# Kernel tuning notes

Hardware: AMD Instinct MI355X
Metric: run time of the kernel (lower is better)

## Reference

```python
import jax, jax.numpy as jnp
import numpy as np

SIZE = 784          # number of MPS sites (pixels)
D = 32              # bond dimension
EMB_D = 2           # local feature dim, embedding x -> [1-x, x]
NUM_LABELS = 10
LABEL_SITE = SIZE // 2
BATCH = 128
INIT_STD = 0.01     # matches default 'random_eye' init


def setup_inputs() -> dict:
    key = jax.random.key(0)
    k1, k2, k3 = jax.random.split(key, 3)
    # raw pixel values in [0,1] so the affine embedding is valid
    batch_input = jax.random.uniform(k1, (BATCH, SIZE), dtype=jnp.float32)
    eye = jnp.eye(D, dtype=jnp.float32)
    # 'random_eye' init: identity (broadcast over site & physical dims) + small noise.
    # Keeps the 784-long matrix chain numerically well-conditioned.
    core_tensors = eye[None, :, None, :] + INIT_STD * jax.random.normal(
        k2, (SIZE, D, EMB_D, D), dtype=jnp.float32)
    label_tensor = eye[:, None, :] + INIT_STD * jax.random.normal(
        k3, (D, NUM_LABELS, D), dtype=jnp.float32)
    return {"batch_input": batch_input,
            "core_tensors": core_tensors,
            "label_tensor": label_tensor}


def _chain_matmul(mats):
    """Ordered product M_0 @ M_1 @ ... @ M_{n-1} via log-depth pairwise tree.
    mats: [B, n, D, D] -> [B, D, D]. n is static, so the Python while is fine."""
    while mats.shape[1] > 1:
        n = mats.shape[1]
        half = n // 2
        prod = jnp.matmul(mats[:, 0:2 * half:2], mats[:, 1:2 * half:2])
        if n % 2:
            prod = jnp.concatenate([prod, mats[:, -1:]], axis=1)
        mats = prod
    return mats[:, 0]


def reference(batch_input, core_tensors, label_tensor):
    # embedding_map: x -> [1-x, x]                                  [B, S, d]
    emb = jnp.stack([1.0 - batch_input, batch_input], axis=-1)
    # _contract_batch_input: per-site matrices M[b,s] = sum_d core[s,:,d,:]*emb[b,s,d]
    mats = jnp.einsum('sadc,bsd->bsac', core_tensors, emb)       # [B, S, D, D]
    left = _chain_matmul(mats[:, :LABEL_SITE])                    # [B, D, D]
    right = _chain_matmul(mats[:, LABEL_SITE:])                   # [B, D, D]
    # periodic bc: out[b,l] = trace(left @ T_l @ right)
    return jnp.einsum('bij,jlk,bki->bl', left, label_tensor, right)  # [B, num_labels]
```

## Files before the change

kernel.cpp:

```cpp
#include <hip/hip_runtime.h>
#include <stdint.h>

typedef float f32x16 __attribute__((ext_vector_type(16)));
typedef short bf16x8 __attribute__((ext_vector_type(8)));
typedef uint32_t u32;
typedef uint32_t u32x4 __attribute__((ext_vector_type(4)));

#define SIZE 784
#define NLBL 10
#define LABEL_SITE 392
#define BATCH 128
#define PRE_ELEMS (SIZE * 2 * 64 * 4)

#if defined(__has_builtin)
#if __has_builtin(__builtin_amdgcn_permlane32_swap)
#define HAVE_PLSWAP 1
#endif
#endif
#ifndef HAVE_PLSWAP
#define HAVE_PLSWAP 0
#endif


__device__ inline u32 cvt_pk(float a, float b) {
  u32 r;
  asm("v_cvt_pk_bf16_f32 %0, %1, %2" : "=v"(r) : "v"(a), "v"(b));
  return r;
}
__device__ inline float lo16f(u32 h) { return __uint_as_float(h << 16); }
__device__ inline float hi16f(u32 h) { return __uint_as_float(h & 0xffff0000u); }

__device__ inline void split_pack(const float s[8], u32 hi[4], u32 lo[4]) {
#pragma unroll
  for (int p = 0; p < 4; ++p) {
    u32 h = cvt_pk(s[2 * p], s[2 * p + 1]);
    hi[p] = h;
    lo[p] = cvt_pk(s[2 * p] - lo16f(h), s[2 * p + 1] - hi16f(h));
  }
}

__device__ inline f32x16 mfma_bb(const u32 (&a)[4], const u32 (&b)[4], f32x16 c) {
  union U { u32 u[4]; bf16x8 v; };
  U A, B;
#pragma unroll
  for (int i = 0; i < 4; ++i) { A.u[i] = a[i]; B.u[i] = b[i]; }
  return __builtin_amdgcn_mfma_f32_32x32x16_bf16(A.v, B.v, c, 0, 0, 0);
}
__device__ inline f32x16 mfma_v4(u32x4 a, const u32 (&b)[4], f32x16 c) {
  union UA { u32x4 u; bf16x8 v; } A; A.u = a;
  union UB { u32 u[4]; bf16x8 v; } B;
#pragma unroll
  for (int i = 0; i < 4; ++i) B.u[i] = b[i];
  return __builtin_amdgcn_mfma_f32_32x32x16_bf16(A.v, B.v, c, 0, 0, 0);
}

__device__ inline f32x16 ident_acc(int lane) {
  const int gam = lane & 31, hib = lane >> 5;
  f32x16 a;
#pragma unroll
  for (int reg = 0; reg < 16; ++reg) {
    int rho = (reg & 3) + 8 * (reg >> 2) + 4 * hib;
    a[reg] = (rho == gam) ? 1.0f : 0.0f;
  }
  return a;
}

__device__ inline int probe_mode(int lane) {
#if HAVE_PLSWAP
  u32 a = (u32)lane, b = (u32)(64 + lane);
  auto r = __builtin_amdgcn_permlane32_swap(a, b, false, false);
  u32 eLo = (u32)(lane + (lane & 32));
  u32 eHi = (u32)(lane + 32 + (lane & 32));
  if (__all(r[0] == eLo) && __all(r[1] == eHi)) return 1;
  if (__all(r[0] == eHi) && __all(r[1] == eLo)) return 2;
#endif
  return 0;
}

template <int MODE>
__device__ inline void build_b(const f32x16& acc, int hib, int t,
                               u32 (&Bh)[4], u32 (&Bl)[4]) {
  float slot[8];
#pragma unroll
  for (int j = 0; j < 4; ++j) {
    const int q1 = 8 * t + j, q2 = q1 + 4;
#if HAVE_PLSWAP
    if (MODE != 0) {
      u32 au = __float_as_uint(acc[q1]), bu = __float_as_uint(acc[q2]);
      auto r = __builtin_amdgcn_permlane32_swap(au, bu, false, false);
      slot[j]     = __uint_as_float(MODE == 1 ? r[0] : r[1]);
      slot[j + 4] = __uint_as_float(MODE == 1 ? r[1] : r[0]);
    } else
#endif
    {
      float z = hib ? acc[q1] : acc[q2];
      float wv = __shfl_xor(z, 32, 64);
      slot[j]     = hib ? wv : acc[q1];
      slot[j + 4] = hib ? acc[q2] : wv;
    }
  }
  split_pack(slot, Bh, Bl);
}

template <int MODE>
__device__ inline f32x16 chain_step(const u32 (&Ah)[2][4], const u32 (&Al)[2][4],
                                    f32x16 acc, int hib) {
  f32x16 r;
#pragma unroll
  for (int q = 0; q < 16; ++q) r[q] = 0.0f;
#pragma unroll
  for (int t = 0; t < 2; ++t) {
    u32 Bh[4], Bl[4];
    build_b<MODE>(acc, hib, t, Bh, Bl);
    r = mfma_bb(Al[t], Bh, r);
    r = mfma_bb(Ah[t], Bl, r);
    r = mfma_bb(Ah[t], Bh, r);
  }
  return r;
}

__device__ inline void store_cd(float* dst, f32x16 acc, int lane) {
  const int gam = lane & 31, hib = lane >> 5;
#pragma unroll
  for (int reg = 0; reg < 16; ++reg) {
    int rho = (reg & 3) + 8 * (reg >> 2) + 4 * hib;
    dst[rho * 32 + gam] = acc[reg];
  }
}

__device__ inline void load_afrag_rm(const float* src, int lane,
                                     u32 (&Ah)[2][4], u32 (&Al)[2][4]) {
  const int row = lane & 31, hb8 = (lane >> 5) * 8;
#pragma unroll
  for (int h = 0; h < 2; ++h) {
    const float* p = src + row * 32 + h * 16 + hb8;
    float4 q0 = *(const float4*)p;
    float4 q1 = *(const float4*)(p + 4);
    float v[8] = {q0.x, q0.y, q0.z, q0.w, q1.x, q1.y, q1.z, q1.w};
    split_pack(v, Ah[h], Al[h]);
  }
}

__global__ __launch_bounds__(256) void mps_precomp(const float* __restrict__ core,
                                                   u32* __restrict__ pc0h,
                                                   u32* __restrict__ pc0l,
                                                   u32* __restrict__ pdh,
                                                   u32* __restrict__ pdl) {
  const int tid = threadIdx.x;
  const int w = tid >> 6, lane = tid & 63;
  const int task = blockIdx.x * 4 + w;
  const int s = task >> 1, t = task & 1;
  const int r = lane & 31, hib = lane >> 5;
  const float* cs = core + (size_t)s * 2048 + r;
  u32 wc0h[4], wc0l[4], wdh[4], wdl[4];
#pragma unroll
  for (int p = 0; p < 4; ++p) {
    const int k0 = 16 * t + 8 * hib + 2 * p;
    float a0 = cs[k0 * 64],       a1 = cs[(k0 + 1) * 64];
    float b0 = cs[k0 * 64 + 32],  b1 = cs[(k0 + 1) * 64 + 32];
    float d0 = b0 - a0, d1 = b1 - a1;
    u32 h = cvt_pk(a0, a1);
    wc0h[p] = h;
    wc0l[p] = cvt_pk(a0 - lo16f(h), a1 - hi16f(h));
    u32 gg = cvt_pk(d0, d1);
    wdh[p] = gg;
    wdl[p] = cvt_pk(d0 - lo16f(gg), d1 - hi16f(gg));
  }
  const size_t base = ((size_t)task * 64 + lane) * 4;
  *(u32x4*)(pc0h + base) = *(u32x4*)wc0h;
  *(u32x4*)(pc0l + base) = *(u32x4*)wc0l;
  *(u32x4*)(pdh  + base) = *(u32x4*)wdh;
  *(u32x4*)(pdl  + base) = *(u32x4*)wdl;
}

template <int MODE>
__device__ void phase1_body(const float* __restrict__ input,
                            const u32* __restrict__ pc0h, const u32* __restrict__ pc0l,
                            const u32* __restrict__ pdh,  const u32* __restrict__ pdl,
                            float* __restrict__ wsA, int nseg, int seglen,
                            int lane, int bi, int g) {
  const int hib = lane >> 5;
  f32x16 acc = ident_acc(lane);
  const int ci0 = g * seglen;
  for (int i = 0; i < seglen; ++i) {
    int s = LABEL_SITE + ci0 + i;
    if (s >= SIZE) s -= SIZE;
    const float x = input[(size_t)bi * SIZE + s];
    f32x16 rc, rd;
#pragma unroll
    for (int q = 0; q < 16; ++q) { rc[q] = 0.0f; rd[q] = 0.0f; }
#pragma unroll
    for (int t = 0; t < 2; ++t) {
      const size_t base = ((size_t)(s * 2 + t) * 64 + lane) * 4;
      u32x4 C0h = *(const u32x4*)(pc0h + base);
      u32x4 C0l = *(const u32x4*)(pc0l + base);
      u32x4 Dh  = *(const u32x4*)(pdh + base);
      u32x4 Dl  = *(const u32x4*)(pdl + base);
      u32 Bh[4], Bl[4];
      build_b<MODE>(acc, hib, t, Bh, Bl);
      rd = mfma_v4(Dl, Bh, rd);
      rd = mfma_v4(Dh, Bl, rd);
      rd = mfma_v4(Dh, Bh, rd);
      rc = mfma_v4(C0l, Bh, rc);
      rc = mfma_v4(C0h, Bl, rc);
      rc = mfma_v4(C0h, Bh, rc);
    }
#pragma unroll
    for (int q = 0; q < 16; ++q) acc[q] = fmaf(x, rd[q], rc[q]);
  }
  store_cd(wsA + ((size_t)bi * nseg + g) * 1024, acc, lane);
}

__global__ __launch_bounds__(256, 4) void mps_phase1(
    const float* __restrict__ input,
    const u32* __restrict__ pc0h, const u32* __restrict__ pc0l,
    const u32* __restrict__ pdh,  const u32* __restrict__ pdl,
    float* __restrict__ wsA, int nseg, int seglen) {
  const int tid = threadIdx.x;
  const int w = tid >> 6, lane = tid & 63;
  const int g = blockIdx.x % nseg, c = blockIdx.x / nseg;
  const int bi = c * 4 + w;
  const int mode = probe_mode(lane);
  if (mode == 1)
    phase1_body<1>(input, pc0h, pc0l, pdh, pdl, wsA, nseg, seglen, lane, bi, g);
  else if (mode == 2)
    phase1_body<2>(input, pc0h, pc0l, pdh, pdl, wsA, nseg, seglen, lane, bi, g);
  else
    phase1_body<0>(input, pc0h, pc0l, pdh, pdl, wsA, nseg, seglen, lane, bi, g);
}

template <int MODE>
__device__ void phase2a_body(const float* __restrict__ wsA, float* __restrict__ wsB,
                             int nseg, int lane, int bi, int gg) {
  f32x16 acc = ident_acc(lane);
  for (int g = gg * 7; g < gg * 7 + 7; ++g) {
    u32 Ah[2][4], Al[2][4];
    load_afrag_rm(wsA + ((size_t)bi * nseg + g) * 1024, lane, Ah, Al);
    acc = chain_step<MODE>(Ah, Al, acc, lane >> 5);
  }
  const int ngroups = nseg / 7;
  store_cd(wsB + ((size_t)bi * ngroups + gg) * 1024, acc, lane);
}

__global__ __launch_bounds__(256) void mps_phase2a(const float* __restrict__ wsA,
                                                   float* __restrict__ wsB,
                                                   int nseg) {
  const int tid = threadIdx.x;
  const int w = tid >> 6, lane = tid & 63;
  const int wid = blockIdx.x * 4 + w;
  const int bi = wid & 127, gg = wid >> 7;
  const int mode = probe_mode(lane);
  if (mode == 1)      phase2a_body<1>(wsA, wsB, nseg, lane, bi, gg);
  else if (mode == 2) phase2a_body<2>(wsA, wsB, nseg, lane, bi, gg);
  else                phase2a_body<0>(wsA, wsB, nseg, lane, bi, gg);
}

template <int MODE>
__device__ void phase2b_body(const float* __restrict__ wsB,
                             const float* __restrict__ label,
                             float* __restrict__ out, int ngroups,
                             int lane, int bi) {
  const int gam = lane & 31, hib = lane >> 5;
  f32x16 acc = ident_acc(lane);
  for (int gg = 0; gg < ngroups; ++gg) {
    u32 Ah[2][4], Al[2][4];
    load_afrag_rm(wsB + ((size_t)bi * ngroups + gg) * 1024, lane, Ah, Al);
    acc = chain_step<MODE>(Ah, Al, acc, hib);
  }
  float part[NLBL];
#pragma unroll
  for (int l = 0; l < NLBL; ++l) part[l] = 0.0f;
#pragma unroll
  for (int reg = 0; reg < 16; ++reg) {
    const int rho = (reg & 3) + 8 * (reg >> 2) + 4 * hib;
    const float wv = acc[reg];
    const float* tp = label + rho * (NLBL * 32) + gam;
#pragma unroll
    for (int l = 0; l < NLBL; ++l) part[l] = fmaf(tp[l * 32], wv, part[l]);
  }
#pragma unroll
  for (int l = 0; l < NLBL; ++l) {
#pragma unroll
    for (int mask = 32; mask >= 1; mask >>= 1)
      part[l] += __shfl_xor(part[l], mask, 64);
  }
  if (lane == 0) {
#pragma unroll
    for (int l = 0; l < NLBL; ++l) out[bi * NLBL + l] = part[l];
  }
}

__global__ __launch_bounds__(256) void mps_phase2b(const float* __restrict__ wsB,
                                                   const float* __restrict__ label,
                                                   float* __restrict__ out,
                                                   int ngroups) {
  const int tid = threadIdx.x;
  const int w = tid >> 6, lane = tid & 63;
  const int bi = blockIdx.x * 4 + w;
  const int mode = probe_mode(lane);
  if (mode == 1)      phase2b_body<1>(wsB, label, out, ngroups, lane, bi);
  else if (mode == 2) phase2b_body<2>(wsB, label, out, ngroups, lane, bi);
  else                phase2b_body<0>(wsB, label, out, ngroups, lane, bi);
}

extern "C" void kernel_launch(void* const* d_in, const int* in_sizes, int n_in,
                              void* d_out, int out_size, void* d_ws, size_t ws_size,
                              hipStream_t stream) {
  const float* input = (const float*)d_in[0];
  const float* core  = (const float*)d_in[1];
  const float* label = (const float*)d_in[2];
  float* out = (float*)d_out;

  u32* pc0h = (u32*)d_ws;
  u32* pc0l = pc0h + PRE_ELEMS;
  u32* pdh  = pc0l + PRE_ELEMS;
  u32* pdl  = pdh + PRE_ELEMS;
  float* wsA = (float*)(pdl + PRE_ELEMS);

  const size_t need112 = ((size_t)4 * PRE_ELEMS + (size_t)BATCH * 112 * 1024 +
                          (size_t)BATCH * 16 * 1024) * 4;
  const int nseg = (ws_size >= need112) ? 112 : 56;
  const int seglen = SIZE / nseg;
  const int ngroups = nseg / 7;
  float* wsB = wsA + (size_t)BATCH * nseg * 1024;

  mps_precomp<<<dim3(392), dim3(256), 0, stream>>>(core, pc0h, pc0l, pdh, pdl);
  mps_phase1<<<dim3(nseg * 32), dim3(256), 0, stream>>>(input, pc0h, pc0l, pdh, pdl,
                                                        wsA, nseg, seglen);
  mps_phase2a<<<dim3(32 * ngroups), dim3(256), 0, stream>>>(wsA, wsB, nseg);
  mps_phase2b<<<dim3(32), dim3(256), 0, stream>>>(wsB, label, out, ngroups);
}
```

Measured before the change: 80.31 us.

## Fuse phase2a/2b into one LDS tree-reduction kernel and prefetch phase1 fragments

Phase 1 now takes the segment length as a compile-time template argument, fully unrolls its loop and double-buffers the per-site fragment loads, so the next site's loads are issued while the current MFMA step runs. The two chain-reduction kernels are merged into a single 512-thread block per batch element. Each of its 8 waves reduces a contiguous run of segments, and the partial products are then combined in a log-depth tree through padded LDS before the label contraction. This removes one kernel launch and the wsB global round trip. In exchange it uses more registers in phase 1, drops the occupancy hint of 4, and leaves only 128 blocks for the final phase.

Measured after the change: 72.30 us. -10.0%, faster.

```diff
diff --git a/kernel.cpp b/kernel.cpp
--- a/kernel.cpp
+++ b/kernel.cpp
@@ -11,6 +11,8 @@
 #define LABEL_SITE 392
 #define BATCH 128
 #define PRE_ELEMS (SIZE * 2 * 64 * 4)
+#define LSTR 33
+#define LSLOT (LSTR * 32)
 
 #if defined(__has_builtin)
 #if __has_builtin(__builtin_amdgcn_permlane32_swap)
@@ -125,6 +127,36 @@
   for (int reg = 0; reg < 16; ++reg) {
     int rho = (reg & 3) + 8 * (reg >> 2) + 4 * hib;
     dst[rho * 32 + gam] = acc[reg];
+  }
+}
+
+__device__ inline void store_cd33(float* dst, f32x16 acc, int lane) {
+  const int gam = lane & 31, hib = lane >> 5;
+#pragma unroll
+  for (int reg = 0; reg < 16; ++reg) {
+    int rho = (reg & 3) + 8 * (reg >> 2) + 4 * hib;
+    dst[rho * LSTR + gam] = acc[reg];
+  }
+}
+__device__ inline f32x16 load_cd33(const float* src, int lane) {
+  const int gam = lane & 31, hib = lane >> 5;
+  f32x16 a;
+#pragma unroll
+  for (int reg = 0; reg < 16; ++reg) {
+    int rho = (reg & 3) + 8 * (reg >> 2) + 4 * hib;
+    a[reg] = src[rho * LSTR + gam];
+  }
+  return a;
+}
+__device__ inline void load_afrag_lds33(const float* src, int lane,
+                                        u32 (&Ah)[2][4], u32 (&Al)[2][4]) {
+  const int row = lane & 31, hb8 = (lane >> 5) * 8;
+#pragma unroll
+  for (int h = 0; h < 2; ++h) {
+    float v[8];
+#pragma unroll
+    for (int j = 0; j < 8; ++j) v[j] = src[row * LSTR + h * 16 + hb8 + j];
+    split_pack(v, Ah[h], Al[h]);
   }
 }
 
@@ -173,134 +205,158 @@
   *(u32x4*)(pdl  + base) = *(u32x4*)wdl;
 }
 
+struct Frags {
+  u32x4 C0h[2], C0l[2], Dh[2], Dl[2];
+  float x;
+};
+
+__device__ inline void load_frags(Frags& F,
+                                  const u32* __restrict__ pc0h, const u32* __restrict__ pc0l,
+                                  const u32* __restrict__ pdh,  const u32* __restrict__ pdl,
+                                  const float* __restrict__ input, int bi, int s, int lane) {
+  F.x = input[(size_t)bi * SIZE + s];
+#pragma unroll
+  for (int t = 0; t < 2; ++t) {
+    const size_t base = ((size_t)(s * 2 + t) * 64 + lane) * 4;
+    F.C0h[t] = *(const u32x4*)(pc0h + base);
+    F.C0l[t] = *(const u32x4*)(pc0l + base);
+    F.Dh[t]  = *(const u32x4*)(pdh + base);
+    F.Dl[t]  = *(const u32x4*)(pdl + base);
+  }
+}
+
 template <int MODE>
+__device__ inline void do_step(f32x16& acc, const Frags& F, int hib) {
+  f32x16 rc, rd;
+#pragma unroll
+  for (int q = 0; q < 16; ++q) { rc[q] = 0.0f; rd[q] = 0.0f; }
+#pragma unroll
+  for (int t = 0; t < 2; ++t) {
+    u32 Bh[4], Bl[4];
+    build_b<MODE>(acc, hib, t, Bh, Bl);
+    rd = mfma_v4(F.Dl[t], Bh, rd);
+    rd = mfma_v4(F.Dh[t], Bl, rd);
+    rd = mfma_v4(F.Dh[t], Bh, rd);
+    rc = mfma_v4(F.C0l[t], Bh, rc);
+    rc = mfma_v4(F.C0h[t], Bl, rc);
+    rc = mfma_v4(F.C0h[t], Bh, rc);
+  }
+#pragma unroll
+  for (int q = 0; q < 16; ++q) acc[q] = fmaf(F.x, rd[q], rc[q]);
+}
+
+template <int SEGLEN, int MODE>
 __device__ void phase1_body(const float* __restrict__ input,
                             const u32* __restrict__ pc0h, const u32* __restrict__ pc0l,
                             const u32* __restrict__ pdh,  const u32* __restrict__ pdl,
-                            float* __restrict__ wsA, int nseg, int seglen,
+                            float* __restrict__ wsA, int nseg,
                             int lane, int bi, int g) {
   const int hib = lane >> 5;
   f32x16 acc = ident_acc(lane);
-  const int ci0 = g * seglen;
-  for (int i = 0; i < seglen; ++i) {
-    int s = LABEL_SITE + ci0 + i;
-    if (s >= SIZE) s -= SIZE;
-    const float x = input[(size_t)bi * SIZE + s];
-    f32x16 rc, rd;
-#pragma unroll
-    for (int q = 0; q < 16; ++q) { rc[q] = 0.0f; rd[q] = 0.0f; }
-#pragma unroll
-    for (int t = 0; t < 2; ++t) {
-      const size_t base = ((size_t)(s * 2 + t) * 64 + lane) * 4;
-      u32x4 C0h = *(const u32x4*)(pc0h + base);
-      u32x4 C0l = *(const u32x4*)(pc0l + base);
-      u32x4 Dh  = *(const u32x4*)(pdh + base);
-      u32x4 Dl  = *(const u32x4*)(pdl + base);
-      u32 Bh[4], Bl[4];
-      build_b<MODE>(acc, hib, t, Bh, Bl);
-      rd = mfma_v4(Dl, Bh, rd);
-      rd = mfma_v4(Dh, Bl, rd);
-      rd = mfma_v4(Dh, Bh, rd);
-      rc = mfma_v4(C0l, Bh, rc);
-      rc = mfma_v4(C0h, Bl, rc);
-      rc = mfma_v4(C0h, Bh, rc);
-    }
-#pragma unroll
-    for (int q = 0; q < 16; ++q) acc[q] = fmaf(x, rd[q], rc[q]);
+  const int ci0 = g * SEGLEN;
+  int s0 = LABEL_SITE + ci0;
+  if (s0 >= SIZE) s0 -= SIZE;
+  Frags FA, FB;
+  load_frags(FA, pc0h, pc0l, pdh, pdl, input, bi, s0, lane);
+#pragma unroll
+  for (int i = 0; i < SEGLEN; ++i) {
+    int sn = LABEL_SITE + ci0 + i + 1;
+    if (sn >= SIZE) sn -= SIZE;
+    if ((i & 1) == 0) {
+      if (i + 1 < SEGLEN) load_frags(FB, pc0h, pc0l, pdh, pdl, input, bi, sn, lane);
+      do_step<MODE>(acc, FA, hib);
+    } else {
+      if (i + 1 < SEGLEN) load_frags(FA, pc0h, pc0l, pdh, pdl, input, bi, sn, lane);
+      do_step<MODE>(acc, FB, hib);
+    }
   }
   store_cd(wsA + ((size_t)bi * nseg + g) * 1024, acc, lane);
 }
 
-__global__ __launch_bounds__(256, 4) void mps_phase1(
+template <int SEGLEN>
+__global__ __launch_bounds__(256) void mps_phase1(
     const float* __restrict__ input,
     const u32* __restrict__ pc0h, const u32* __restrict__ pc0l,
     const u32* __restrict__ pdh,  const u32* __restrict__ pdl,
-    float* __restrict__ wsA, int nseg, int seglen) {
+    float* __restrict__ wsA, int nseg) {
   const int tid = threadIdx.x;
   const int w = tid >> 6, lane = tid & 63;
   const int g = blockIdx.x % nseg, c = blockIdx.x / nseg;
   const int bi = c * 4 + w;
   const int mode = probe_mode(lane);
   if (mode == 1)
-    phase1_body<1>(input, pc0h, pc0l, pdh, pdl, wsA, nseg, seglen, lane, bi, g);
+    phase1_body<SEGLEN, 1>(input, pc0h, pc0l, pdh, pdl, wsA, nseg, lane, bi, g);
   else if (mode == 2)
-    phase1_body<2>(input, pc0h, pc0l, pdh, pdl, wsA, nseg, seglen, lane, bi, g);
+    phase1_body<SEGLEN, 2>(input, pc0h, pc0l, pdh, pdl, wsA, nseg, lane, bi, g);
   else
-    phase1_body<0>(input, pc0h, pc0l, pdh, pdl, wsA, nseg, seglen, lane, bi, g);
+    phase1_body<SEGLEN, 0>(input, pc0h, pc0l, pdh, pdl, wsA, nseg, lane, bi, g);
 }
 
 template <int MODE>
-__device__ void phase2a_body(const float* __restrict__ wsA, float* __restrict__ wsB,
-                             int nseg, int lane, int bi, int gg) {
+__device__ void phase2_body(const float* __restrict__ wsA,
+                            const float* __restrict__ label,
+                            float* __restrict__ out, int nseg,
+                            int lane, int w, int bi, float* lds) {
+  const int per = nseg / 8;
   f32x16 acc = ident_acc(lane);
-  for (int g = gg * 7; g < gg * 7 + 7; ++g) {
+  for (int g = w * per; g < (w + 1) * per; ++g) {
     u32 Ah[2][4], Al[2][4];
     load_afrag_rm(wsA + ((size_t)bi * nseg + g) * 1024, lane, Ah, Al);
     acc = chain_step<MODE>(Ah, Al, acc, lane >> 5);
   }
-  const int ngroups = nseg / 7;
-  store_cd(wsB + ((size_t)bi * ngroups + gg) * 1024, acc, lane);
-}
-
-__global__ __launch_bounds__(256) void mps_phase2a(const float* __restrict__ wsA,
-                                                   float* __restrict__ wsB,
-                                                   int nseg) {
+  store_cd33(lds + w * LSLOT, acc, lane);
+  __syncthreads();
+  f32x16 na;
+#pragma unroll
+  for (int lvl = 4; lvl >= 1; lvl >>= 1) {
+    const bool act = (w < lvl);
+    if (act) {
+      f32x16 a = load_cd33(lds + (2 * w) * LSLOT, lane);
+      u32 Ah[2][4], Al[2][4];
+      load_afrag_lds33(lds + (2 * w + 1) * LSLOT, lane, Ah, Al);
+      na = chain_step<MODE>(Ah, Al, a, lane >> 5);
+    }
+    __syncthreads();
+    if (act) store_cd33(lds + w * LSLOT, na, lane);
+    __syncthreads();
+  }
+  if (w == 0) {
+    const int gam = lane & 31, hib = lane >> 5;
+    float part[NLBL];
+#pragma unroll
+    for (int l = 0; l < NLBL; ++l) part[l] = 0.0f;
+#pragma unroll
+    for (int reg = 0; reg < 16; ++reg) {
+      const int rho = (reg & 3) + 8 * (reg >> 2) + 4 * hib;
+      const float wv = na[reg];
+      const float* tp = label + rho * (NLBL * 32) + gam;
+#pragma unroll
+      for (int l = 0; l < NLBL; ++l) part[l] = fmaf(tp[l * 32], wv, part[l]);
+    }
+#pragma unroll
+    for (int l = 0; l < NLBL; ++l) {
+#pragma unroll
+      for (int mask = 32; mask >= 1; mask >>= 1)
+        part[l] += __shfl_xor(part[l], mask, 64);
+    }
+    if (lane == 0) {
+#pragma unroll
+      for (int l = 0; l < NLBL; ++l) out[bi * NLBL + l] = part[l];
+    }
+  }
+}
+
+__global__ __launch_bounds__(512) void mps_phase2(const float* __restrict__ wsA,
+                                                  const float* __restrict__ label,
+                                                  float* __restrict__ out, int nseg) {
+  __shared__ float lds[8 * LSLOT];
   const int tid = threadIdx.x;
   const int w = tid >> 6, lane = tid & 63;
-  const int wid = blockIdx.x * 4 + w;
-  const int bi = wid & 127, gg = wid >> 7;
+  const int bi = blockIdx.x;
   const int mode = probe_mode(lane);
-  if (mode == 1)      phase2a_body<1>(wsA, wsB, nseg, lane, bi, gg);
-  else if (mode == 2) phase2a_body<2>(wsA, wsB, nseg, lane, bi, gg);
-  else                phase2a_body<0>(wsA, wsB, nseg, lane, bi, gg);
-}
-
-template <int MODE>
-__device__ void phase2b_body(const float* __restrict__ wsB,
-                             const float* __restrict__ label,
-                             float* __restrict__ out, int ngroups,
-                             int lane, int bi) {
-  const int gam = lane & 31, hib = lane >> 5;
-  f32x16 acc = ident_acc(lane);
-  for (int gg = 0; gg < ngroups; ++gg) {
-    u32 Ah[2][4], Al[2][4];
-    load_afrag_rm(wsB + ((size_t)bi * ngroups + gg) * 1024, lane, Ah, Al);
-    acc = chain_step<MODE>(Ah, Al, acc, hib);
-  }
-  float part[NLBL];
-#pragma unroll
-  for (int l = 0; l < NLBL; ++l) part[l] = 0.0f;
-#pragma unroll
-  for (int reg = 0; reg < 16; ++reg) {
-    const int rho = (reg & 3) + 8 * (reg >> 2) + 4 * hib;
-    const float wv = acc[reg];
-    const float* tp = label + rho * (NLBL * 32) + gam;
-#pragma unroll
-    for (int l = 0; l < NLBL; ++l) part[l] = fmaf(tp[l * 32], wv, part[l]);
-  }
-#pragma unroll
-  for (int l = 0; l < NLBL; ++l) {
-#pragma unroll
-    for (int mask = 32; mask >= 1; mask >>= 1)
-      part[l] += __shfl_xor(part[l], mask, 64);
-  }
-  if (lane == 0) {
-#pragma unroll
-    for (int l = 0; l < NLBL; ++l) out[bi * NLBL + l] = part[l];
-  }
-}
-
-__global__ __launch_bounds__(256) void mps_phase2b(const float* __restrict__ wsB,
-                                                   const float* __restrict__ label,
-                                                   float* __restrict__ out,
-                                                   int ngroups) {
-  const int tid = threadIdx.x;
-  const int w = tid >> 6, lane = tid & 63;
-  const int bi = blockIdx.x * 4 + w;
-  const int mode = probe_mode(lane);
-  if (mode == 1)      phase2b_body<1>(wsB, label, out, ngroups, lane, bi);
-  else if (mode == 2) phase2b_body<2>(wsB, label, out, ngroups, lane, bi);
-  else                phase2b_body<0>(wsB, label, out, ngroups, lane, bi);
+  if (mode == 1)      phase2_body<1>(wsA, label, out, nseg, lane, w, bi, lds);
+  else if (mode == 2) phase2_body<2>(wsA, label, out, nseg, lane, w, bi, lds);
+  else                phase2_body<0>(wsA, label, out, nseg, lane, w, bi, lds);
 }
 
 extern "C" void kernel_launch(void* const* d_in, const int* in_sizes, int n_in,
@@ -317,16 +373,15 @@
   u32* pdl  = pdh + PRE_ELEMS;
   float* wsA = (float*)(pdl + PRE_ELEMS);
 
-  const size_t need112 = ((size_t)4 * PRE_ELEMS + (size_t)BATCH * 112 * 1024 +
-                          (size_t)BATCH * 16 * 1024) * 4;
+  const size_t need112 = ((size_t)4 * PRE_ELEMS + (size_t)BATCH * 112 * 1024) * 4;
   const int nseg = (ws_size >= need112) ? 112 : 56;
-  const int seglen = SIZE / nseg;
-  const int ngroups = nseg / 7;
-  float* wsB = wsA + (size_t)BATCH * nseg * 1024;
 
   mps_precomp<<<dim3(392), dim3(256), 0, stream>>>(core, pc0h, pc0l, pdh, pdl);
-  mps_phase1<<<dim3(nseg * 32), dim3(256), 0, stream>>>(input, pc0h, pc0l, pdh, pdl,
-                                                        wsA, nseg, seglen);
-  mps_phase2a<<<dim3(32 * ngroups), dim3(256), 0, stream>>>(wsA, wsB, nseg);
-  mps_phase2b<<<dim3(32), dim3(256), 0, stream>>>(wsB, label, out, ngroups);
-}
+  if (nseg == 112)
+    mps_phase1<7><<<dim3(112 * 32), dim3(256), 0, stream>>>(input, pc0h, pc0l, pdh, pdl,
+                                                            wsA, 112);
+  else
+    mps_phase1<14><<<dim3(56 * 32), dim3(256), 0, stream>>>(input, pc0h, pc0l, pdh, pdl,
+                                                            wsA, 56);
+  mps_phase2<<<dim3(BATCH), dim3(512), 0, stream>>>(wsA, label, out, nseg);
+}
```

## Precompute pairwise site products to halve sequential chain steps in phase1

Applied to the files above, without the earlier changes.

A new precompute kernel multiplies adjacent site cores into four 32x32 pair matrices (CC, CD, DC, DD) per site pair and stores them as bf16 hi/lo splits. Phase1 then advances the accumulated product two sites per step, using 24 MFMAs against these four pair matrices and combining them with the bilinear weights x0 and x1. This halves the length of the serial dependency chain per segment but doubles the MFMA work per site and the table bytes loaded per step. The segment count also changes from 112 to 98, and the occupancy hint of 4 blocks per CU is dropped from phase1's launch bounds.

New measurement: 97.12 us. +20.9%, slower.

```diff
diff --git a/kernel.cpp b/kernel.cpp
--- a/kernel.cpp
+++ b/kernel.cpp
@@ -10,7 +10,8 @@
 #define NLBL 10
 #define LABEL_SITE 392
 #define BATCH 128
-#define PRE_ELEMS (SIZE * 2 * 64 * 4)
+#define NPAIR 392
+#define TBL_U32 ((size_t)NPAIR * 4096)
 
 #if defined(__has_builtin)
 #if __has_builtin(__builtin_amdgcn_permlane32_swap)
@@ -21,6 +22,12 @@
 #define HAVE_PLSWAP 0
 #endif
 
+
+__device__ inline int site_of(int ci) {
+  int s = LABEL_SITE + ci;
+  if (s >= SIZE) s -= SIZE;
+  return s;
+}
 
 __device__ inline u32 cvt_pk(float a, float b) {
   u32 r;
@@ -141,92 +148,109 @@
   }
 }
 
-__global__ __launch_bounds__(256) void mps_precomp(const float* __restrict__ core,
-                                                   u32* __restrict__ pc0h,
-                                                   u32* __restrict__ pc0l,
-                                                   u32* __restrict__ pdh,
-                                                   u32* __restrict__ pdl) {
+__device__ inline f32x16 chain6(u32x4 Th0, u32x4 Tl0, u32x4 Th1, u32x4 Tl1,
+                                const u32 (&B0h)[4], const u32 (&B0l)[4],
+                                const u32 (&B1h)[4], const u32 (&B1l)[4],
+                                const f32x16& z) {
+  f32x16 r = mfma_v4(Tl0, B0h, z);
+  r = mfma_v4(Th0, B0l, r);
+  r = mfma_v4(Th0, B0h, r);
+  r = mfma_v4(Tl1, B1h, r);
+  r = mfma_v4(Th1, B1l, r);
+  r = mfma_v4(Th1, B1h, r);
+  return r;
+}
+
+__global__ __launch_bounds__(256) void mps_precomp_pairs(const float* __restrict__ core,
+                                                         u32* __restrict__ table) {
+  __shared__ float CA[32 * 33], DA[32 * 33], CB[32 * 33], DB[32 * 33];
   const int tid = threadIdx.x;
   const int w = tid >> 6, lane = tid & 63;
-  const int task = blockIdx.x * 4 + w;
-  const int s = task >> 1, t = task & 1;
+  const int p = blockIdx.x;
+  const int sA = site_of(2 * p), sB = site_of(2 * p + 1);
+  for (int f = tid; f < 2048; f += 256) {
+    int r = f & 31, e = (f >> 5) & 1, k = f >> 6;
+    float vA = core[(size_t)sA * 2048 + f];
+    float vB = core[(size_t)sB * 2048 + f];
+    if (e == 0) { CA[r * 33 + k] = vA; CB[r * 33 + k] = vB; }
+    else        { DA[r * 33 + k] = vA; DB[r * 33 + k] = vB; }
+  }
+  __syncthreads();
+  for (int f = tid; f < 1024; f += 256) {
+    int r = f & 31, k = f >> 5;
+    DA[r * 33 + k] -= CA[r * 33 + k];
+    DB[r * 33 + k] -= CB[r * 33 + k];
+  }
+  __syncthreads();
+  const float* Lm = (w < 2) ? CB : DB;
+  const float* Rm = (w & 1) ? DA : CA;
   const int r = lane & 31, hib = lane >> 5;
-  const float* cs = core + (size_t)s * 2048 + r;
-  u32 wc0h[4], wc0l[4], wdh[4], wdl[4];
-#pragma unroll
-  for (int p = 0; p < 4; ++p) {
-    const int k0 = 16 * t + 8 * hib + 2 * p;
-    float a0 = cs[k0 * 64],       a1 = cs[(k0 + 1) * 64];
-    float b0 = cs[k0 * 64 + 32],  b1 = cs[(k0 + 1) * 64 + 32];
-    float d0 = b0 - a0, d1 = b1 - a1;
-    u32 h = cvt_pk(a0, a1);
-    wc0h[p] = h;
-    wc0l[p] = cvt_pk(a0 - lo16f(h), a1 - hi16f(h));
-    u32 gg = cvt_pk(d0, d1);
-    wdh[p] = gg;
-    wdl[p] = cvt_pk(d0 - lo16f(gg), d1 - hi16f(gg));
-  }
-  const size_t base = ((size_t)task * 64 + lane) * 4;
-  *(u32x4*)(pc0h + base) = *(u32x4*)wc0h;
-  *(u32x4*)(pc0l + base) = *(u32x4*)wc0l;
-  *(u32x4*)(pdh  + base) = *(u32x4*)wdh;
-  *(u32x4*)(pdl  + base) = *(u32x4*)wdl;
+  float Lr[32];
+#pragma unroll
+  for (int j = 0; j < 32; ++j) Lr[j] = Lm[r * 33 + j];
+#pragma unroll
+  for (int t = 0; t < 2; ++t) {
+    float o[8];
+#pragma unroll
+    for (int jj = 0; jj < 8; ++jj) {
+      const int k = 16 * t + 8 * hib + jj;
+      float s = 0.0f;
+#pragma unroll
+      for (int j = 0; j < 32; ++j) s = fmaf(Lr[j], Rm[j * 33 + k], s);
+      o[jj] = s;
+    }
+    u32 hi[4], lo[4];
+    split_pack(o, hi, lo);
+    const size_t base = (size_t)p * 4096 + (size_t)(w * 4 + t * 2) * 256 + lane * 4;
+    *(u32x4*)(table + base) = *(u32x4*)hi;
+    *(u32x4*)(table + base + 256) = *(u32x4*)lo;
+  }
 }
 
 template <int MODE>
 __device__ void phase1_body(const float* __restrict__ input,
-                            const u32* __restrict__ pc0h, const u32* __restrict__ pc0l,
-                            const u32* __restrict__ pdh,  const u32* __restrict__ pdl,
-                            float* __restrict__ wsA, int nseg, int seglen,
+                            const u32* __restrict__ table,
+                            float* __restrict__ wsA, int nseg, int pairs,
                             int lane, int bi, int g) {
   const int hib = lane >> 5;
   f32x16 acc = ident_acc(lane);
-  const int ci0 = g * seglen;
-  for (int i = 0; i < seglen; ++i) {
-    int s = LABEL_SITE + ci0 + i;
-    if (s >= SIZE) s -= SIZE;
-    const float x = input[(size_t)bi * SIZE + s];
-    f32x16 rc, rd;
-#pragma unroll
-    for (int q = 0; q < 16; ++q) { rc[q] = 0.0f; rd[q] = 0.0f; }
-#pragma unroll
-    for (int t = 0; t < 2; ++t) {
-      const size_t base = ((size_t)(s * 2 + t) * 64 + lane) * 4;
-      u32x4 C0h = *(const u32x4*)(pc0h + base);
-      u32x4 C0l = *(const u32x4*)(pc0l + base);
-      u32x4 Dh  = *(const u32x4*)(pdh + base);
-      u32x4 Dl  = *(const u32x4*)(pdl + base);
-      u32 Bh[4], Bl[4];
-      build_b<MODE>(acc, hib, t, Bh, Bl);
-      rd = mfma_v4(Dl, Bh, rd);
-      rd = mfma_v4(Dh, Bl, rd);
-      rd = mfma_v4(Dh, Bh, rd);
-      rc = mfma_v4(C0l, Bh, rc);
-      rc = mfma_v4(C0h, Bl, rc);
-      rc = mfma_v4(C0h, Bh, rc);
-    }
-#pragma unroll
-    for (int q = 0; q < 16; ++q) acc[q] = fmaf(x, rd[q], rc[q]);
+  f32x16 z16;
+#pragma unroll
+  for (int q = 0; q < 16; ++q) z16[q] = 0.0f;
+  const int ci0 = g * 2 * pairs;
+  for (int i = 0; i < pairs; ++i) {
+    const int ci = ci0 + 2 * i;
+    const float x0 = input[(size_t)bi * SIZE + site_of(ci)];
+    const float x1 = input[(size_t)bi * SIZE + site_of(ci + 1)];
+    const u32* tb = table + (size_t)(g * pairs + i) * 4096 + lane * 4;
+    u32x4 T[16];
+#pragma unroll
+    for (int q = 0; q < 16; ++q) T[q] = *(const u32x4*)(tb + q * 256);
+    u32 B0h[4], B0l[4], B1h[4], B1l[4];
+    build_b<MODE>(acc, hib, 0, B0h, B0l);
+    build_b<MODE>(acc, hib, 1, B1h, B1l);
+    f32x16 rcc = chain6(T[0],  T[1],  T[2],  T[3],  B0h, B0l, B1h, B1l, z16);
+    f32x16 rcd = chain6(T[4],  T[5],  T[6],  T[7],  B0h, B0l, B1h, B1l, z16);
+    f32x16 rdc = chain6(T[8],  T[9],  T[10], T[11], B0h, B0l, B1h, B1l, z16);
+    f32x16 rdd = chain6(T[12], T[13], T[14], T[15], B0h, B0l, B1h, B1l, z16);
+#pragma unroll
+    for (int q = 0; q < 16; ++q)
+      acc[q] = fmaf(x1, fmaf(x0, rdd[q], rdc[q]), fmaf(x0, rcd[q], rcc[q]));
   }
   store_cd(wsA + ((size_t)bi * nseg + g) * 1024, acc, lane);
 }
 
-__global__ __launch_bounds__(256, 4) void mps_phase1(
-    const float* __restrict__ input,
-    const u32* __restrict__ pc0h, const u32* __restrict__ pc0l,
-    const u32* __restrict__ pdh,  const u32* __restrict__ pdl,
-    float* __restrict__ wsA, int nseg, int seglen) {
+__global__ __launch_bounds__(256) void mps_phase1(
+    const float* __restrict__ input, const u32* __restrict__ table,
+    float* __restrict__ wsA, int nseg, int pairs) {
   const int tid = threadIdx.x;
   const int w = tid >> 6, lane = tid & 63;
   const int g = blockIdx.x % nseg, c = blockIdx.x / nseg;
   const int bi = c * 4 + w;
   const int mode = probe_mode(lane);
-  if (mode == 1)
-    phase1_body<1>(input, pc0h, pc0l, pdh, pdl, wsA, nseg, seglen, lane, bi, g);
-  else if (mode == 2)
-    phase1_body<2>(input, pc0h, pc0l, pdh, pdl, wsA, nseg, seglen, lane, bi, g);
-  else
-    phase1_body<0>(input, pc0h, pc0l, pdh, pdl, wsA, nseg, seglen, lane, bi, g);
+  if (mode == 1)      phase1_body<1>(input, table, wsA, nseg, pairs, lane, bi, g);
+  else if (mode == 2) phase1_body<2>(input, table, wsA, nseg, pairs, lane, bi, g);
+  else                phase1_body<0>(input, table, wsA, nseg, pairs, lane, bi, g);
 }
 
 template <int MODE>
@@ -311,22 +335,18 @@
   const float* label = (const float*)d_in[2];
   float* out = (float*)d_out;
 
-  u32* pc0h = (u32*)d_ws;
-  u32* pc0l = pc0h + PRE_ELEMS;
-  u32* pdh  = pc0l + PRE_ELEMS;
-  u32* pdl  = pdh + PRE_ELEMS;
-  float* wsA = (float*)(pdl + PRE_ELEMS);
-
-  const size_t need112 = ((size_t)4 * PRE_ELEMS + (size_t)BATCH * 112 * 1024 +
-                          (size_t)BATCH * 16 * 1024) * 4;
-  const int nseg = (ws_size >= need112) ? 112 : 56;
-  const int seglen = SIZE / nseg;
+  u32* table = (u32*)d_ws;
+  float* wsA = (float*)(table + TBL_U32);
+
+  const size_t need98 = (TBL_U32 + (size_t)BATCH * 98 * 1024 +
+                         (size_t)BATCH * 14 * 1024) * 4;
+  const int nseg = (ws_size >= need98) ? 98 : 56;
+  const int pairs = (SIZE / nseg) / 2;
   const int ngroups = nseg / 7;
   float* wsB = wsA + (size_t)BATCH * nseg * 1024;
 
-  mps_precomp<<<dim3(392), dim3(256), 0, stream>>>(core, pc0h, pc0l, pdh, pdl);
-  mps_phase1<<<dim3(nseg * 32), dim3(256), 0, stream>>>(input, pc0h, pc0l, pdh, pdl,
-                                                        wsA, nseg, seglen);
+  mps_precomp_pairs<<<dim3(NPAIR), dim3(256), 0, stream>>>(core, table);
+  mps_phase1<<<dim3(nseg * 32), dim3(256), 0, stream>>>(input, table, wsA, nseg, pairs);
   mps_phase2a<<<dim3(32 * ngroups), dim3(256), 0, stream>>>(wsA, wsB, nseg);
   mps_phase2b<<<dim3(32), dim3(256), 0, stream>>>(wsB, label, out, ngroups);
 }
```
